# Optimization experiments

Hardware: AMD Instinct MI355X
Metric: run time of the kernel (lower is better)

The kernel has to match this reference:

```python
import jax, jax.numpy as jnp
import numpy as np

B, L, H, W = 16, 4096, 64, 64
SEQ = 1024  # target_sequence_length (hardcoded in the torch module)
SP = 32     # sqrt(SEQ)


def _conv1d(x, w, b, pad):
    y = jax.lax.conv_general_dilated(x, w, (1,), [(pad, pad)],
                                     dimension_numbers=('NCH', 'OIH', 'NCH'))
    return y + b[None, :, None]


def _conv2d(x, w, b, pad, groups=1):
    y = jax.lax.conv_general_dilated(x, w, (1, 1), [(pad, pad)] * 2,
                                     feature_group_count=groups,
                                     dimension_numbers=('NCHW', 'OIHW', 'NCHW'))
    return y + b[None, :, None, None]


def _forward(us_input, img_input, us_w1, us_b1, us_w2, us_b2, us_w3, us_b3,
             aff_w, aff_w_high, aff_thr, img_w1, img_b1, img_w2, img_b2, img_w3, img_b3,
             db_qkv_w, db_qkv_b, db_dw_w, db_dw_b, db_proj_w, db_proj_b,
             db_fc_w, db_fc_b, db_dep_w, db_dep_b, db_temp,
             ca_qkv_w, ca_qkv_b, ca_out_w, ca_out_b,
             tf_ch1_w, tf_ch1_b, tf_ch2_w, tf_ch2_b,
             tf_sp1_w, tf_sp1_b, tf_sp2_w, tf_sp2_b, cls_w, cls_b):
    b = us_input.shape[0]
    # ---- ultrasound 1D conv branch ----
    x = us_input.transpose(0, 2, 1)                    # [B,1,L]
    x = jax.nn.relu(_conv1d(x, us_w1, us_b1, 1))
    x = jax.nn.relu(_conv1d(x, us_w2, us_b2, 1))
    x = jax.nn.relu(_conv1d(x, us_w3, us_b3, 1))
    us_feat = x.transpose(0, 2, 1)                     # [B,L,64]
    # ---- adaptive frequency filtering (training-mode high-freq mask included) ----
    n = us_feat.shape[1]
    xf = jnp.fft.rfft(us_feat, axis=1, norm='ortho')   # [B,Nf,64] complex
    w_c = aff_w[:, 0] + 1j * aff_w[:, 1]
    xw = xf * w_c
    energy = jnp.sum(jnp.abs(xf) ** 2, axis=-1)        # [B,Nf]
    med = jnp.median(energy.reshape(b, -1), axis=1, keepdims=True)
    ne = energy / (med + 1e-6)
    hard = (ne > aff_thr).astype(jnp.float32)
    mask = jax.lax.stop_gradient(hard - aff_thr) + aff_thr  # straight-through threshold
    wh_c = aff_w_high[:, 0] + 1j * aff_w_high[:, 1]
    xw = xw + (xf * mask[..., None]) * wh_c
    us_feat = jnp.fft.irfft(xw, n=n, axis=1, norm='ortho')  # [B,L,64]
    # ---- image 2D conv branch ----
    y = jax.nn.relu(_conv2d(img_input, img_w1, img_b1, 1))
    y = jax.nn.relu(_conv2d(y, img_w2, img_b2, 1))
    y = jax.nn.relu(_conv2d(y, img_w3, img_b3, 1))     # [B,64,H,W]
    # ---- dual-branch feature fusion block ----
    hgt, wid = y.shape[2], y.shape[3]
    hw = hgt * wid
    qkv = jnp.einsum('oi,bihw->bohw', db_qkv_w, y) + db_qkv_b[None, :, None, None]
    qkv = _conv2d(qkv, db_dw_w, db_dw_b, 1, groups=192)      # depthwise (3x3x3 conv @ D=1 -> center 3x3)
    # convolutional branch: faithful row-major reshape as in torch
    f_all = qkv.reshape(b, hw, 12, 16).transpose(0, 2, 1, 3)  # [B,12,HW,16]
    f_all = jnp.einsum('oi,bink->bonk', db_fc_w, f_all) + db_fc_b[None, :, None, None]
    f_conv = f_all.transpose(0, 3, 1, 2).reshape(b, 144, hgt, wid)
    out_conv = _conv2d(f_conv, db_dep_w, db_dep_b, 1, groups=16)  # [B,64,H,W]
    # channel attention branch
    q, k, v = jnp.split(qkv, 3, axis=1)
    q = q.reshape(b, 4, 16, hw)
    k = k.reshape(b, 4, 16, hw)
    v = v.reshape(b, 4, 16, hw)
    q = q / jnp.maximum(jnp.linalg.norm(q, axis=-1, keepdims=True), 1e-12)
    k = k / jnp.maximum(jnp.linalg.norm(k, axis=-1, keepdims=True), 1e-12)
    attn = jax.nn.softmax(jnp.einsum('bhcn,bhdn->bhcd', q, k) * db_temp, axis=-1)
    out = jnp.einsum('bhcd,bhdn->bhcn', attn, v).reshape(b, 64, hgt, wid)
    out = jnp.einsum('oi,bihw->bohw', db_proj_w, out) + db_proj_b[None, :, None, None]
    img_feat = (out + out_conv).reshape(b, 64, hw).transpose(0, 2, 1)  # [B,HW,64]
    # ---- adaptive avg pool to SEQ (lengths divide evenly) ----
    us_red = us_feat.transpose(0, 2, 1).reshape(b, 64, SEQ, -1).mean(-1).transpose(0, 2, 1)
    img_red = img_feat.transpose(0, 2, 1).reshape(b, 64, SEQ, -1).mean(-1).transpose(0, 2, 1)
    # ---- cross-modal attention (shared qkv/out projections) ----
    def heads(t):
        u = (jnp.einsum('bli,oi->blo', t, ca_qkv_w) + ca_qkv_b).reshape(b, SEQ, 4, 3, 16)
        return (u[:, :, :, 0].transpose(0, 2, 1, 3),
                u[:, :, :, 1].transpose(0, 2, 1, 3),
                u[:, :, :, 2].transpose(0, 2, 1, 3))
    q1, k1, v1 = heads(us_red)
    q2, k2, v2 = heads(img_red)
    scale = 1.0 / jnp.sqrt(jnp.float32(16.0))
    a1 = jax.nn.softmax(jnp.einsum('bhqd,bhkd->bhqk', q1, k2) * scale, axis=-1)
    a2 = jax.nn.softmax(jnp.einsum('bhqd,bhkd->bhqk', q2, k1) * scale, axis=-1)
    o1 = jnp.einsum('bhqk,bhkd->bhqd', a1, v2).transpose(0, 2, 1, 3).reshape(b, SEQ, 64)
    o2 = jnp.einsum('bhqk,bhkd->bhqd', a2, v1).transpose(0, 2, 1, 3).reshape(b, SEQ, 64)
    o1 = jnp.einsum('bli,oi->blo', o1, ca_out_w) + ca_out_b
    o2 = jnp.einsum('bli,oi->blo', o2, ca_out_w) + ca_out_b
    t1 = o1.transpose(0, 2, 1).reshape(b, 64, SP, SP)
    t2 = o2.transpose(0, 2, 1).reshape(b, 64, SP, SP)
    # ---- modal fusion attention (channel + spatial gating) ----
    ch_pool = jnp.stack([t1.mean((2, 3)), t1.max((2, 3)), t2.mean((2, 3)), t2.max((2, 3))], axis=1)  # [B,4,64]
    c1 = _conv1d(ch_pool, tf_ch1_w, tf_ch1_b, 1)      # [B,1,64]
    c2 = _conv1d(ch_pool, tf_ch2_w, tf_ch2_b, 1)
    ch_stack = jax.nn.softmax(jnp.stack([c1, c2], 0), axis=0)      # [2,B,1,64]
    ch_stack = ch_stack.transpose(0, 1, 3, 2)[..., None]           # [2,B,64,1,1]
    sp_pool = jnp.concatenate([t1.mean(1, keepdims=True), t1.max(1, keepdims=True),
                               t2.mean(1, keepdims=True), t2.max(1, keepdims=True)], axis=1)
    s1 = _conv2d(sp_pool, tf_sp1_w, tf_sp1_b, 3)
    s2 = _conv2d(sp_pool, tf_sp2_w, tf_sp2_b, 3)
    sp_stack = jax.nn.softmax(jnp.stack([s1, s2], 0), axis=0)      # [2,B,1,SP,SP]
    att = ch_stack + sp_stack + 1.0                                # [2,B,64,SP,SP]
    fuse = att[0] * t1 + att[1] * t2
    logits = fuse.mean((2, 3)) @ cls_w.T + cls_b
    return jax.nn.softmax(logits, axis=1)


def setup_inputs() -> dict:
    key = jax.random.key(0)
    ks = iter(jax.random.split(key, 64))
    def rn(shape, s=0.2):
        return jax.random.normal(next(ks), shape, dtype=jnp.float32) * s
    d = {
        'us_input': jax.random.normal(next(ks), (B, L, 1), dtype=jnp.float32),
        'img_input': jax.random.normal(next(ks), (B, 3, H, W), dtype=jnp.float32),
        'us_w1': rn((16, 1, 3)), 'us_b1': rn((16,), 0.02),
        'us_w2': rn((32, 16, 3)), 'us_b2': rn((32,), 0.02),
        'us_w3': rn((64, 32, 3)), 'us_b3': rn((64,), 0.02),
        'aff_w': rn((64, 2), 0.02), 'aff_w_high': rn((64, 2), 0.02),
        'aff_thr': jax.random.uniform(next(ks), (1,), dtype=jnp.float32),
        'img_w1': rn((16, 3, 3, 3)), 'img_b1': rn((16,), 0.02),
        'img_w2': rn((32, 16, 3, 3)), 'img_b2': rn((32,), 0.02),
        'img_w3': rn((64, 32, 3, 3)), 'img_b3': rn((64,), 0.02),
        'db_qkv_w': rn((192, 64), 0.1), 'db_qkv_b': rn((192,), 0.02),
        'db_dw_w': rn((192, 1, 3, 3)), 'db_dw_b': rn((192,), 0.02),
        'db_proj_w': rn((64, 64), 0.1), 'db_proj_b': rn((64,), 0.02),
        'db_fc_w': rn((9, 12), 0.1), 'db_fc_b': rn((9,), 0.02),
        'db_dep_w': rn((64, 9, 3, 3), 0.1), 'db_dep_b': rn((64,), 0.02),
        'db_temp': jnp.ones((4, 1, 1), dtype=jnp.float32),
        'ca_qkv_w': rn((192, 64), 0.1), 'ca_qkv_b': rn((192,), 0.02),
        'ca_out_w': rn((64, 64), 0.1), 'ca_out_b': rn((64,), 0.02),
        'tf_ch1_w': rn((1, 4, 3)), 'tf_ch1_b': rn((1,), 0.02),
        'tf_ch2_w': rn((1, 4, 3)), 'tf_ch2_b': rn((1,), 0.02),
        'tf_sp1_w': rn((1, 4, 7, 7)), 'tf_sp1_b': rn((1,), 0.02),
        'tf_sp2_w': rn((1, 4, 7, 7)), 'tf_sp2_b': rn((1,), 0.02),
        'cls_w': rn((9, 64), 0.1), 'cls_b': rn((9,), 0.02),
    }
    return d


def reference(us_input, img_input, us_w1, us_b1, us_w2, us_b2, us_w3, us_b3,
              aff_w, aff_w_high, aff_thr, img_w1, img_b1, img_w2, img_b2, img_w3, img_b3,
              db_qkv_w, db_qkv_b, db_dw_w, db_dw_b, db_proj_w, db_proj_b,
              db_fc_w, db_fc_b, db_dep_w, db_dep_b, db_temp,
              ca_qkv_w, ca_qkv_b, ca_out_w, ca_out_b,
              tf_ch1_w, tf_ch1_b, tf_ch2_w, tf_ch2_b,
              tf_sp1_w, tf_sp1_b, tf_sp2_w, tf_sp2_b, cls_w, cls_b):
    return _forward(us_input, img_input, us_w1, us_b1, us_w2, us_b2, us_w3, us_b3,
                    aff_w, aff_w_high, aff_thr, img_w1, img_b1, img_w2, img_b2, img_w3, img_b3,
                    db_qkv_w, db_qkv_b, db_dw_w, db_dw_b, db_proj_w, db_proj_b,
                    db_fc_w, db_fc_b, db_dep_w, db_dep_b, db_temp,
                    ca_qkv_w, ca_qkv_b, ca_out_w, ca_out_b,
                    tf_ch1_w, tf_ch1_b, tf_ch2_w, tf_ch2_b,
                    tf_sp1_w, tf_sp1_b, tf_sp2_w, tf_sp2_b, cls_w, cls_b)
```

## Files before the change

kernel.cpp:

```cpp
#include <hip/hip_runtime.h>

typedef float v2f __attribute__((ext_vector_type(2)));

static constexpr size_t O_SMALL   = 0;
static constexpr size_t O_US3     = 3145728;
static constexpr size_t O_XF      = 7340032;
static constexpr size_t O_USFILT  = 11536384;
static constexpr size_t O_ENERGY  = 15730688;
static constexpr size_t O_MED     = 15764480;
static constexpr size_t O_NRM     = 15765504;
static constexpr size_t O_ATTNS   = 15767552;
static constexpr size_t O_CHPOOL  = 15783936;
static constexpr size_t O_CHW     = 15788032;
static constexpr size_t O_SPPOOL  = 15790080;
static constexpr size_t O_SPW     = 15855616;
static constexpr size_t O_QKV     = 15888384;
static constexpr size_t O_QKVDW   = 28471296;
static constexpr size_t O_OUTCONV = 41054208;
static constexpr size_t CA_USRED = 0, CA_IMGRED = 1, CA_Q1 = 2, CA_K1 = 3, CA_V1 = 4,
                        CA_Q2 = 5, CA_K2 = 6, CA_V2 = 7, CA_O1 = 8, CA_O2 = 9,
                        CA_T1 = 10, CA_T2 = 11;


template<int Ci, int Co>
// ... 56 lines not shown
    for (int i = tid; i < Ci * (TY + 2) * 64; i += 256) {
        int x  = i & 63;
        int ry = (i >> 6) % (TY + 2);
        int ci = i / ((TY + 2) * 64);
        int gy = y0 - 1 + ry;
        lds[ci][ry][x + 1] = (gy >= 0 && gy < 64) ? inb[ci * 4096 + gy * 64 + x] : 0.f;
    }
    for (int r = tid; r < Ci * (TY + 2); r += 256) {
        int ry = r % (TY + 2), ci = r / (TY + 2);
        lds[ci][ry][0] = 0.f; lds[ci][ry][65] = 0.f;
    }
    __syncthreads();
    int co   = tid / (TY * G);
    int ysub = (tid / G) % TY;
    int x0   = (tid % G) * N;
    float acc[N];
    float bias = bs[co];
#pragma unroll
    for (int j = 0; j < N; ++j) acc[j] = bias;
    const float* wb = w + co * Ci * 9;
    for (int ci = 0; ci < Ci; ++ci) {
        float wr[9];
#pragma unroll
        for (int k = 0; k < 9; ++k) wr[k] = wb[ci * 9 + k];
#pragma unroll
        for (int dy = 0; dy < 3; ++dy) {
            const float* lr = &lds[ci][ysub + dy][x0];
            float a = lr[0], bb = lr[1];
#pragma unroll
            for (int j = 0; j < N; ++j) {
                float cc = lr[2 + j];
                acc[j] += wr[dy * 3] * a + wr[dy * 3 + 1] * bb + wr[dy * 3 + 2] * cc;
                a = bb; bb = cc;
            }
        }
    }
    float* ob = out + ((size_t)b * Co + co) * 4096 + (y0 + ysub) * 64 + x0;
#pragma unroll
    for (int j = 0; j < N; ++j) ob[j] = fmaxf(acc[j], 0.f);
}

__device__ __forceinline__ void fft4096_r4_sb(float2* A, int tid)
{
    int Ns = 1;
    for (int s = 0; s < 6; ++s) {
        float cfac = -0.25f / (float)Ns;
        float2 va[4][4];
#pragma unroll
        for (int r = 0; r < 4; ++r) {
            int j = (r << 8) + tid;
            va[r][0] = A[j];
            va[r][1] = A[j + 1024];
            va[r][2] = A[j + 2048];
            va[r][3] = A[j + 3072];
        }
        __syncthreads();
#pragma unroll
        for (int r = 0; r < 4; ++r) {
            int j = (r << 8) + tid;
            int jm = j & (Ns - 1);
            float rev = (float)jm * cfac;
            float s1 = __builtin_amdgcn_sinf(rev);
            float c1 = __builtin_amdgcn_cosf(rev);
            float c2 = c1 * c1 - s1 * s1, s2 = 2.f * c1 * s1;
            float c3 = c2 * c1 - s2 * s1, s3 = c2 * s1 + s2 * c1;
            float2 v0 = va[r][0], v1 = va[r][1], v2 = va[r][2], v3 = va[r][3];
            float2 u1 = make_float2(v1.x * c1 - v1.y * s1, v1.x * s1 + v1.y * c1);
            float2 u2 = make_float2(v2.x * c2 - v2.y * s2, v2.x * s2 + v2.y * c2);
            float2 u3 = make_float2(v3.x * c3 - v3.y * s3, v3.x * s3 + v3.y * c3);
            float t0x = v0.x + u2.x, t0y = v0.y + u2.y;
            float t1x = v0.x - u2.x, t1y = v0.y - u2.y;
            float t2x = u1.x + u3.x, t2y = u1.y + u3.y;
            float t3x = u1.x - u3.x, t3y = u1.y - u3.y;
            int base = ((j - jm) << 2) + jm;
            A[base]          = make_float2(t0x + t2x, t0y + t2y);
            A[base + Ns]     = make_float2(t1x + t3y, t1y - t3x);
            A[base + 2 * Ns] = make_float2(t0x - t2x, t0y - t2y);
            A[base + 3 * Ns] = make_float2(t1x - t3y, t1y + t3x);
        }
        __syncthreads();
        Ns <<= 2;
    }
}

__device__ __forceinline__ void fft_fwd_body(char* smem_raw, int row,
    const float* __restrict__ us3, float* __restrict__ xf)
{
    float2* A = (float2*)smem_raw;
    int tid = threadIdx.x;
    const float* x = us3 + (size_t)row * 4096;
    for (int r = 0; r < 16; ++r) {
        int i = (r << 8) + tid;
        A[i] = make_float2(x[i], 0.f);
    }
    __syncthreads();
    fft4096_r4_sb(A, tid);
    float* out = xf + (size_t)row * 4098;
    for (int r = 0; r < 9; ++r) {
        int f = (r << 8) + tid;
        if (f < 2049) {
            out[2 * f]     = A[f].x * (1.f / 64.f);
            out[2 * f + 1] = A[f].y * (1.f / 64.f);
        }
    }
}

__device__ __forceinline__ void energy_body(int bid,
    const float* __restrict__ xf, float* __restrict__ energy)
{
    int idx = bid * 256 + threadIdx.x;
    if (idx >= 16 * 2049) return;
    int b = idx / 2049, f = idx % 2049;
    const float* p = xf + (size_t)b * 64 * 4098 + 2 * f;
    float e = 0.f;
    for (int ch = 0; ch < 64; ++ch) {
        float re = p[0], im = p[1];
        e += re * re + im * im;
        p += 4098;
    }
    energy[idx] = e;
}

__device__ __forceinline__ void median_body(char* smem_raw, int b,
    const float* __restrict__ energy, float* __restrict__ med)
{
    float* s = (float*)smem_raw;
    int tid = threadIdx.x;
    for (int r = 0; r < 16; ++r) {
        int i = (r << 8) + tid;
        s[i] = (i < 2049) ? energy[b * 2049 + i] : 3.0e38f;
    }
    __syncthreads();
    for (int k = 2; k <= 4096; k <<= 1) {
        for (int j = k >> 1; j > 0; j >>= 1) {
            for (int r = 0; r < 16; ++r) {
                int i = (r << 8) + tid;
                int ixj = i ^ j;
                if (ixj > i) {
                    bool up = ((i & k) == 0);
                    float a = s[i], bb = s[ixj];
                    if ((a > bb) == up) { s[i] = bb; s[ixj] = a; }
                }
            }
            __syncthreads();
        }
    }
    if (tid == 0) med[b] = s[1024];
}

__device__ __forceinline__ void filter_ifft_body(char* smem_raw, int row,
    const float* __restrict__ xf, const float* __restrict__ energy,
    const float* __restrict__ med, const float* __restrict__ aff_w,
    const float* __restrict__ aff_wh, const float* __restrict__ thr_p,
    float* __restrict__ us_filt)
{
    float2* A = (float2*)smem_raw;
    int b = row >> 6, ch = row & 63;
    int tid = threadIdx.x;
    float thr = thr_p[0];
    float mden = med[b] + 1e-6f;
    float w0r = aff_w[2 * ch], w0i = aff_w[2 * ch + 1];
    float whr = aff_wh[2 * ch], whi = aff_wh[2 * ch + 1];
    const float* X = xf + (size_t)row * 4098;
    const float* E = energy + b * 2049;
    for (int r = 0; r < 9; ++r) {
        int f = (r << 8) + tid;
        if (f < 2049) {
            float re = X[2 * f], im = X[2 * f + 1];
            float mask = (E[f] / mden > thr) ? 1.f : 0.f;
            float wr = w0r + mask * whr;
            float wi = w0i + mask * whi;
            float xr = re * wr - im * wi;
            float xi = re * wi + im * wr;
            A[f] = make_float2(xr, -xi);
            if (f >= 1 && f <= 2047) A[4096 - f] = make_float2(xr, xi);
        }
    }
    __syncthreads();
    fft4096_r4_sb(A, tid);
    float* out = us_filt + (size_t)row * 4096;
    for (int r = 0; r < 16; ++r) {
        int i = (r << 8) + tid;
        out[i] = A[i].x * (1.f / 64.f);
    }
}

__device__ __forceinline__ void qkv1x1_body(int bid, const float* __restrict__ y,
    const float* __restrict__ w, const float* __restrict__ bs, float* __restrict__ out)
{
    int oc = bid & 3;
    int pc = (bid >> 2) & 15;
    int b  = bid >> 6;
    int p = pc * 256 + threadIdx.x;
    const float* inb = y + (size_t)b * 262144 + p;
    v2f reg[32];
#pragma unroll
    for (int ci = 0; ci < 32; ++ci) {
        v2f r; r.x = inb[(2 * ci) * 4096]; r.y = inb[(2 * ci + 1) * 4096];
        reg[ci] = r;
    }
    float* ob = out + (size_t)b * 786432 + (size_t)oc * 48 * 4096 + p;
    for (int o = 0; o < 48; ++o) {
        const v2f* wr = (const v2f*)(w + (oc * 48 + o) * 64);
        v2f s2 = {0.f, 0.f};
#pragma unroll
        for (int ci = 0; ci < 32; ++ci) s2 = wr[ci] * reg[ci] + s2;
        ob[o * 4096] = bs[oc * 48 + o] + s2.x + s2.y;
    }
}

__device__ __forceinline__ void dwconv_body(int bid, const float* __restrict__ in,
    const float* __restrict__ w, const float* __restrict__ bs, float* __restrict__ out)
{
    int idx = bid * 256 + threadIdx.x;
    int x = idx & 63, yy = (idx >> 6) & 63;
    int c = (idx >> 12) % 192;
    const float* p = in + idx;
    const float* wp = w + c * 9;
    float acc = bs[c];
    bool ym = yy > 0, yp = yy < 63, xm = x > 0, xp = x < 63;
    float s = wp[4] * p[0];
    if (ym) { s += wp[1] * p[-64]; if (xm) s += wp[0] * p[-65]; if (xp) s += wp[2] * p[-63]; }
    if (xm) s += wp[3] * p[-1];
    if (xp) s += wp[5] * p[1];
    if (yp) { s += wp[7] * p[64];  if (xm) s += wp[6] * p[63];  if (xp) s += wp[8] * p[65]; }
    out[idx] = acc + s;
}

__device__ __forceinline__ void fc_body(int bid, const float* __restrict__ qkv_dw,
    const float* __restrict__ fw, const float* __restrict__ fb, float* __restrict__ fcv)
{
    int idx = bid * 256 + threadIdx.x;
    int k = idx & 15;
    int p = (idx >> 4) & 4095;
    int b = idx >> 16;
    const float* base = qkv_dw + (size_t)b * 786432;
    float u[12];
#pragma unroll
    for (int i = 0; i < 12; ++i) u[i] = base[p * 192 + i * 16 + k];
#pragma unroll
    for (int o = 0; o < 9; ++o) {
        float s = fb[o];
#pragma unroll
        for (int i = 0; i < 12; ++i) s += fw[o * 12 + i] * u[i];
        fcv[(((size_t)b * 16 + k) * 9 + o) * 4096 + p] = s;
    }
}

__device__ __forceinline__ void depconv2_body(char* smem_raw, int bid,
    const float* __restrict__ fcv, const float* __restrict__ w,
    const float* __restrict__ bs, float* __restrict__ out)
{
    auto lds = (float(*)[10][66])smem_raw;
    int band = bid & 7;
    int g    = (bid >> 3) & 15;
    int b    = bid >> 7;
    int y0 = band * 8;
    int tid = threadIdx.x;
    const float* inb = fcv + ((size_t)(b * 16 + g) * 9) * 4096;
    for (int i = tid; i < 9 * 10 * 64; i += 256) {
        int x  = i & 63;
        int ry = (i >> 6) % 10;
        int ci = i / 640;
        int gy = y0 - 1 + ry;
        lds[ci][ry][x + 1] = (gy >= 0 && gy < 64) ? inb[ci * 4096 + gy * 64 + x] : 0.f;
    }
    for (int i = tid; i < 90; i += 256) {
        int ry = i % 10, ci = i / 10;
        lds[ci][ry][0] = 0.f; lds[ci][ry][65] = 0.f;
    }
    __syncthreads();
    int co   = tid >> 6;
    int ysub = (tid >> 3) & 7;
    int x0   = (tid & 7) * 8;
    int ocg  = g * 4 + co;
    float acc[8];
    float bias = bs[ocg];
#pragma unroll
    for (int j = 0; j < 8; ++j) acc[j] = bias;
    const float* wb = w + ocg * 81;
    for (int ci = 0; ci < 9; ++ci) {
        float wr[9];
#pragma unroll
        for (int k = 0; k < 9; ++k) wr[k] = wb[ci * 9 + k];
#pragma unroll
        for (int dy = 0; dy < 3; ++dy) {
            const float* lr = &lds[ci][ysub + dy][x0];
            float a = lr[0], bb = lr[1];
#pragma unroll
            for (int j = 0; j < 8; ++j) {
                float cc = lr[2 + j];
                acc[j] += wr[dy * 3] * a + wr[dy * 3 + 1] * bb + wr[dy * 3 + 2] * cc;
                a = bb; bb = cc;
            }
        }
    }
    float* ob = out + ((size_t)b * 64 + ocg) * 4096 + (y0 + ysub) * 64 + x0;
#pragma unroll
    for (int j = 0; j < 8; ++j) ob[j] = acc[j];
}

__device__ __forceinline__ void qknorm_body(char* smem_raw, int row,
    const float* __restrict__ qkv_dw, float* __restrict__ nrm)
{
    float* red = (float*)smem_raw;
    int which = row >> 10;
    int r = row & 1023;
    int b = r >> 6, hd = r & 63;
    const float* p = qkv_dw + ((size_t)b * 192 + which * 64 + hd) * 4096;
    float s = 0.f;
    for (int i = threadIdx.x; i < 4096; i += 256) { float v = p[i]; s += v * v; }
    red[threadIdx.x] = s;
    __syncthreads();
    for (int st = 128; st > 0; st >>= 1) {
        if (threadIdx.x < st) red[threadIdx.x] += red[threadIdx.x + st];
        __syncthreads();
    }
    if (threadIdx.x == 0) nrm[row] = sqrtf(red[0]);
}

__device__ __forceinline__ void chan_attn_part_body(char* smem_raw, int blk,
    const float* __restrict__ qkv_dw, float* __restrict__ part)
{
    auto Qs  = (float(*)[130])smem_raw;
    auto Ks2 = (float(*)[130])(smem_raw + 16 * 130 * 4);
    int nc = blk & 7;
    int bh = blk >> 3;
    int b = bh >> 2, h = bh & 3;
    int c = threadIdx.x >> 4, d = threadIdx.x & 15;
    const float* qbase = qkv_dw + ((size_t)b * 192 + h * 16) * 4096 + nc * 512;
    const float* kbase = qkv_dw + ((size_t)b * 192 + 64 + h * 16) * 4096 + nc * 512;
    float s = 0.f;
    for (int n0 = 0; n0 < 512; n0 += 128) {
        __syncthreads();
        for (int r = 0; r < 8; ++r) {
            int i = (r << 8) + threadIdx.x;
// ... 15 lines not shown
    int b  = bid >> 4;
    int wave = threadIdx.x >> 6, lane = threadIdx.x & 63;
    int c = rg * 4 + wave;
    const float* p1 = t1 + ((size_t)b * 64 + c) * 1024;
    const float* p2 = t2 + ((size_t)b * 64 + c) * 1024;
    float m1 = 0.f, x1 = -3e38f, m2 = 0.f, x2 = -3e38f;
#pragma unroll
    for (int i = 0; i < 16; ++i) {
        int p = lane + i * 64;
        float a = p1[p], bb = p2[p];
        m1 += a; x1 = fmaxf(x1, a);
        m2 += bb; x2 = fmaxf(x2, bb);
    }
    for (int off = 32; off > 0; off >>= 1) {
        m1 += __shfl_xor(m1, off);
        x1 = fmaxf(x1, __shfl_xor(x1, off));
        m2 += __shfl_xor(m2, off);
        x2 = fmaxf(x2, __shfl_xor(x2, off));
    }
    if (lane == 0) {
        chpool[b * 256 + c]       = m1 * (1.f / 1024.f);
        chpool[b * 256 + 64 + c]  = x1;
        chpool[b * 256 + 128 + c] = m2 * (1.f / 1024.f);
        chpool[b * 256 + 192 + c] = x2;
    }
}

__device__ __forceinline__ void sppool_body(int bid, const float* __restrict__ t1,
    const float* __restrict__ t2, float* __restrict__ sppool)
{
    int b = bid >> 2;
    int p = (bid & 3) * 256 + threadIdx.x;
    float m1 = 0.f, x1 = -3e38f, m2 = 0.f, x2 = -3e38f;
    const float* p1 = t1 + (size_t)b * 65536 + p;
    const float* p2 = t2 + (size_t)b * 65536 + p;
    for (int c = 0; c < 64; ++c) {
        float a = p1[c * 1024], bb = p2[c * 1024];
        m1 += a; x1 = fmaxf(x1, a);
        m2 += bb; x2 = fmaxf(x2, bb);
    }
    sppool[b * 4096 + p]        = m1 * (1.f / 64.f);
    sppool[b * 4096 + 1024 + p] = x1;
    sppool[b * 4096 + 2048 + p] = m2 * (1.f / 64.f);
    sppool[b * 4096 + 3072 + p] = x2;
}

__device__ __forceinline__ void chgate_body(int b, const float* __restrict__ chpool,
    const float* __restrict__ w1, const float* __restrict__ b1,
    const float* __restrict__ w2, const float* __restrict__ b2, float* __restrict__ chw)
{
    int c = threadIdx.x;
    if (c >= 64) return;
    float a1 = b1[0], a2 = b2[0];
    for (int ic = 0; ic < 4; ++ic) {
        const float* cp = chpool + b * 256 + ic * 64;
        for (int d = -1; d <= 1; ++d) {
            int cc = c + d;
            if (cc >= 0 && cc < 64) {
                a1 += w1[ic * 3 + d + 1] * cp[cc];
                a2 += w2[ic * 3 + d + 1] * cp[cc];
            }
        }
    }
    float mx = fmaxf(a1, a2);
    float e1 = __expf(a1 - mx), e2 = __expf(a2 - mx);
    float inv = 1.f / (e1 + e2);
    chw[b * 64 + c]        = e1 * inv;
    chw[1024 + b * 64 + c] = e2 * inv;
}

__device__ __forceinline__ void spgate_body(int bid, const float* __restrict__ sppool,
    const float* __restrict__ w1, const float* __restrict__ b1,
    const float* __restrict__ w2, const float* __restrict__ b2, float* __restrict__ spw)
{
    int idx = bid * 256 + threadIdx.x;
    int p = idx & 1023;
    int b = idx >> 10;
    int y = p >> 5, x = p & 31;
    float a1 = b1[0], a2 = b2[0];
    for (int ic = 0; ic < 4; ++ic) {
        const float* sp = sppool + b * 4096 + ic * 1024;
        for (int dy = -3; dy <= 3; ++dy) {
            int yy = y + dy;
            if (yy < 0 || yy > 31) continue;
            for (int dx = -3; dx <= 3; ++dx) {
                int xx = x + dx;
                if (xx < 0 || xx > 31) continue;
                float v = sp[yy * 32 + xx];
                int wi = ic * 49 + (dy + 3) * 7 + (dx + 3);
                a1 += w1[wi] * v;
                a2 += w2[wi] * v;
            }
        }
    }
    float mx = fmaxf(a1, a2);
    float e1 = __expf(a1 - mx), e2 = __expf(a2 - mx);
    float inv = 1.f / (e1 + e2);
    spw[idx]         = e1 * inv;
    spw[16384 + idx] = e2 * inv;
}


__global__ __launch_bounds__(256) void s1_kernel(const float* us_in, const float* uw, const float* ub,
    float* uo, const float* iin, const float* iw, const float* ib, float* io)
{
    __shared__ __align__(16) char smem[3168];
    if (blockIdx.x < 512) conv1d3_body<1, 16>(smem, blockIdx.x, us_in, uw, ub, uo);
    else                  conv2d3_body<3, 16, 2>(smem, blockIdx.x - 512, iin, iw, ib, io);
}

__global__ __launch_bounds__(256) void s2_kernel(const float* ui, const float* uw, const float* ub,
    float* uo, const float* ii, const float* iw, const float* ib, float* io)
{
    __shared__ __align__(16) char smem[16896];
    if (blockIdx.x < 512) conv1d3_body<16, 32>(smem, blockIdx.x, ui, uw, ub, uo);
    else                  conv2d3_body<16, 32, 2>(smem, blockIdx.x - 512, ii, iw, ib, io);
}

__global__ __launch_bounds__(256) void s3_kernel(const float* ui, const float* uw, const float* ub,
    float* uo, const float* ii, const float* iw, const float* ib, float* io)
{
    __shared__ __align__(16) char smem[33792];
    if (blockIdx.x < 512) conv1d3_body<32, 64>(smem, blockIdx.x, ui, uw, ub, uo);
    else                  conv2d3_body<32, 64, 2>(smem, blockIdx.x - 512, ii, iw, ib, io);
}

__global__ __launch_bounds__(256) void s4_kernel(const float* us3, float* xf,
    const float* y, const float* qw, const float* qb, float* qkv)
{
    __shared__ __align__(16) char smem[32768];
    if (blockIdx.x < 1024) fft_fwd_body(smem, blockIdx.x, us3, xf);
    else                   qkv1x1_body(blockIdx.x - 1024, y, qw, qb, qkv);
}

__global__ __launch_bounds__(256) void s5_kernel(const float* qkv, const float* dww,
    const float* dwb, float* qkv_dw, const float* xf, float* energy)
{
    if (blockIdx.x < 49152) dwconv_body(blockIdx.x, qkv, dww, dwb, qkv_dw);
    else                    energy_body(blockIdx.x - 49152, xf, energy);
}

__global__ __launch_bounds__(256) void s6_kernel(const float* qkv_dw, const float* fw,
    const float* fb, float* fcv, const float* energy, float* med, float* part)
{
    __shared__ __align__(16) char smem[16640];
    if (blockIdx.x < 4096)      fc_body(blockIdx.x, qkv_dw, fw, fb, fcv);
    else if (blockIdx.x < 4112) median_body(smem, blockIdx.x - 4096, energy, med);
    else                        chan_attn_part_body(smem, blockIdx.x - 4112, qkv_dw, part);
}

__global__ __launch_bounds__(256) void s7_kernel(const float* fcv, const float* dw,
    const float* db, float* out_conv, const float* qkv_dw, float* nrm,
    const float* xf, const float* energy, const float* med, const float* aw,
    const float* awh, const float* thr, float* us_filt)
{
    __shared__ __align__(16) char smem[32768];
    if (blockIdx.x < 2048)      depconv2_body(smem, blockIdx.x, fcv, dw, db, out_conv);
    else if (blockIdx.x < 4096) qknorm_body(smem, blockIdx.x - 2048, qkv_dw, nrm);
    else                        filter_ifft_body(smem, blockIdx.x - 4096, xf, energy, med, aw, awh, thr, us_filt);
}

__global__ __launch_bounds__(256) void zero_kernel(float* o1t, float* o2t, float* lsg)
{
    int idx = blockIdx.x * 256 + threadIdx.x;
    if (idx < 1048576) { o1t[idx] = 0.f; o2t[idx] = 0.f; }
    if (idx < 131072) lsg[idx] = 0.f;
}

__global__ __launch_bounds__(256) void s16_kernel(const float* t1, const float* t2,
    float* chpool, float* sppool)
{
    if (blockIdx.x < 256) chpool2_body(blockIdx.x, t1, t2, chpool);
    else                  sppool_body(blockIdx.x - 256, t1, t2, sppool);
}

__global__ __launch_bounds__(256) void s17_kernel(const float* sppool, const float* sw1,
    const float* sb1, const float* sw2, const float* sb2, float* spw,
    const float* chpool, const float* cw1, const float* cb1, const float* cw2,
    const float* cb2, float* chw)
{
    if (blockIdx.x < 64) spgate_body(blockIdx.x, sppool, sw1, sb1, sw2, sb2, spw);
    else                 chgate_body(blockIdx.x - 64, chpool, cw1, cb1, cw2, cb2, chw);
}

__global__ __launch_bounds__(256) void chan_attn_merge_kernel(
    const float* __restrict__ part, const float* __restrict__ nrm,
    const float* __restrict__ temp, float* __restrict__ attn_s)
{
    int bh = blockIdx.x;
    int b = bh >> 2, h = bh & 3;
    int c = threadIdx.x >> 4, d = threadIdx.x & 15;
    float s = 0.f;
#pragma unroll
    for (int i = 0; i < 8; ++i) s += part[(size_t)(bh * 8 + i) * 256 + threadIdx.x];
    float nq = fmaxf(nrm[b * 64 + h * 16 + c], 1e-12f);
    float nk = fmaxf(nrm[1024 + b * 64 + h * 16 + d], 1e-12f);
    s = s / (nq * nk) * temp[h];
    __shared__ float S[16][17];
    S[c][d] = s;
    __syncthreads();
    if (threadIdx.x < 16) {
        int cc = threadIdx.x;
        float mx = -3e30f;
        for (int dd = 0; dd < 16; ++dd) mx = fmaxf(mx, S[cc][dd]);
        float sm = 0.f;
        float e[16];
        for (int dd = 0; dd < 16; ++dd) { e[dd] = __expf(S[cc][dd] - mx); sm += e[dd]; }
        float inv = 1.f / sm;
        float* dst = attn_s + (size_t)bh * 256 + cc * 16;
        for (int dd = 0; dd < 16; ++dd) dst[dd] = e[dd] * inv;
    }
}


__global__ __launch_bounds__(256, 2) void attnproj_kernel(const float* __restrict__ attn_s,
    const float* __restrict__ qkv_dw, const float* __restrict__ outconv,
    const float* __restrict__ pw, const float* __restrict__ pb, float* __restrict__ img_feat)
{
    int blk = blockIdx.x;
    int oc = blk & 1;
    int pc = (blk >> 1) & 15;
    int b  = blk >> 5;
    int n = pc * 256 + threadIdx.x;
    const float* vb = qkv_dw + ((size_t)b * 192 + 128) * 4096 + n;
    v2f v[32];
#pragma unroll
    for (int i = 0; i < 32; ++i) {
        v2f r; r.x = vb[(2 * i) * 4096]; r.y = vb[(2 * i + 1) * 4096];
        v[i] = r;
    }
    const float* ab = attn_s + (size_t)b * 1024;
    for (int h = 0; h < 4; ++h) {
        v2f tmp[8];
#pragma unroll
        for (int c2 = 0; c2 < 8; ++c2) {
            v2f s2a = {0.f, 0.f}, s2b = {0.f, 0.f};
            const v2f* r0 = (const v2f*)(ab + (h * 16 + 2 * c2) * 16);
            const v2f* r1 = (const v2f*)(ab + (h * 16 + 2 * c2 + 1) * 16);
#pragma unroll
            for (int d2 = 0; d2 < 8; ++d2) {
                s2a = r0[d2] * v[h * 8 + d2] + s2a;
                s2b = r1[d2] * v[h * 8 + d2] + s2b;
            }
            v2f t; t.x = s2a.x + s2a.y; t.y = s2b.x + s2b.y;
            tmp[c2] = t;
        }
#pragma unroll
        for (int c2 = 0; c2 < 8; ++c2) v[h * 8 + c2] = tmp[c2];
    }
    float* ofb = img_feat + (size_t)b * 262144 + (size_t)oc * 32 * 4096 + n;
    const float* ocb = outconv + (size_t)b * 262144 + (size_t)oc * 32 * 4096 + n;
    for (int o = 0; o < 32; ++o) {
        const v2f* wr = (const v2f*)(pw + (oc * 32 + o) * 64);
        v2f s2 = {0.f, 0.f};
#pragma unroll
        for (int c2 = 0; c2 < 32; ++c2) s2 = wr[c2] * v[c2] + s2;
        ofb[o * 4096] = pb[oc * 32 + o] + ocb[o * 4096] + s2.x + s2.y;
    }
}

__global__ __launch_bounds__(256) void poolred_kernel(const float* __restrict__ us_filt,
    const float* __restrict__ img_feat, float* __restrict__ us_redT, float* __restrict__ img_redT)
{
    int idx = blockIdx.x * 256 + threadIdx.x;
    int s4 = idx & 1023;
    int c = (idx >> 10) & 63;
    int b = (idx >> 16) & 15;
    int m = idx >> 20;
    const float* in = (m ? img_feat : us_filt) + ((size_t)b * 64 + c) * 4096 + s4 * 4;
    float4 v4 = *(const float4*)in;
    float v = 0.25f * (v4.x + v4.y + v4.z + v4.w);
    (m ? img_redT : us_redT)[((size_t)b * 64 + c) * 1024 + s4] = v;
}

__global__ __launch_bounds__(256, 2) void caqkv2_kernel(const float* __restrict__ us_redT,
    const float* __restrict__ img_redT, const float* __restrict__ qw, const float* __restrict__ qb,
    float* __restrict__ q1, float* __restrict__ k1, float* __restrict__ v1,
    float* __restrict__ q2, float* __restrict__ k2, float* __restrict__ v2)
{
    int blk = blockIdx.x;
    int h  = blk & 3;
    int pc = (blk >> 2) & 3;
    int b  = (blk >> 4) & 15;
    int m  = blk >> 8;
    int l = pc * 256 + threadIdx.x;
    const float* in = (m ? img_redT : us_redT) + (size_t)b * 65536 + l;
    v2f reg[32];
#pragma unroll
    for (int i = 0; i < 32; ++i) {
        v2f r; r.x = in[(2 * i) * 1024]; r.y = in[(2 * i + 1) * 1024];
        reg[i] = r;
    }
    size_t rowoff = ((size_t)(b * 4 + h) * 1024 + l) * 16;
    float* dst[3] = { (m ? q2 : q1) + rowoff, (m ? k2 : k1) + rowoff, (m ? v2 : v1) + rowoff };
#pragma unroll
    for (int which = 0; which < 3; ++which) {
        float* dp = dst[which];
        for (int d = 0; d < 16; ++d) {
            int o = h * 48 + which * 16 + d;
            const v2f* wr = (const v2f*)(qw + o * 64);
            v2f s2 = {0.f, 0.f};
#pragma unroll
            for (int i = 0; i < 32; ++i) s2 = wr[i] * reg[i] + s2;
            dp[d] = qb[o] + s2.x + s2.y;
        }
    }
}

__global__ __launch_bounds__(256) void kmax_kernel(const float* __restrict__ k1,
    const float* __restrict__ k2, float* __restrict__ kmax)
{
    int unit = blockIdx.x;
    int h = unit & 3, m = (unit >> 2) & 1, b = unit >> 3;
    const float* K = m ? k1 : k2;
    const float* Kb = K + (size_t)(b * 4 + h) * 16384;
    int tid = threadIdx.x;
    float mx = 0.f;
#pragma unroll
    for (int j = 0; j < 4; ++j) {
        const float* kp = Kb + (size_t)(tid + 256 * j) * 16;
        float s = 0.f;
#pragma unroll
        for (int d = 0; d < 16; ++d) s += kp[d] * kp[d];
        mx = fmaxf(mx, s);
    }
    for (int off = 32; off > 0; off >>= 1) mx = fmaxf(mx, __shfl_xor(mx, off));
    __shared__ float red[4];
    if ((tid & 63) == 0) red[tid >> 6] = mx;
    __syncthreads();
    if (tid == 0) {
        float r = fmaxf(fmaxf(red[0], red[1]), fmaxf(red[2], red[3]));
        kmax[unit] = sqrtf(r);
    }
}

__global__ __launch_bounds__(256, 2) void cross_attn9_kernel(
    const float* __restrict__ q1, const float* __restrict__ k1, const float* __restrict__ v1,
    const float* __restrict__ q2, const float* __restrict__ k2, const float* __restrict__ v2,
    const float* __restrict__ kmax, float* __restrict__ ls_glob,
    float* __restrict__ o1t, float* __restrict__ o2t)
{
    int blk  = blockIdx.x;
    int kt   = blk & 7;
    int unit = blk >> 3;
    int h = unit & 3;
    int m = (unit >> 2) & 1;
    int b = unit >> 3;
    const float* Q = m ? q2 : q1;
    const float* K = m ? k1 : k2;
    const float* V = m ? v1 : v2;
    const float* Qb = Q + (size_t)(b * 4 + h) * 16384;
    const float* Kb = K + (size_t)(b * 4 + h) * 16384 + kt * 128 * 16;
    const float* Vb = V + (size_t)(b * 4 + h) * 16384 + kt * 128 * 16;
    int tid = threadIdx.x;
    const float SC = 0.25f * 1.44269504088896340736f;
    float km = kmax[unit];
    v2f qr[4][8], acc[4][8];
    float M[4], ls[4];
#pragma unroll
    for (int j = 0; j < 4; ++j) {
        const v2f* qp = (const v2f*)(Qb + (size_t)(tid + 256 * j) * 16);
        v2f qs2 = {0.f, 0.f};
#pragma unroll
        for (int i = 0; i < 8; ++i) {
            v2f q = qp[i];
            qs2 = q * q + qs2;
            qr[j][i] = q * SC;
        }
        M[j] = sqrtf(qs2.x + qs2.y) * km * SC;
        ls[j] = 0.f;
#pragma unroll
        for (int i = 0; i < 8; ++i) acc[j][i] = (v2f){0.f, 0.f};
    }
    __shared__ float Ks[64 * 16];
    __shared__ float Vs[64 * 16];
    for (int t0 = 0; t0 < 128; t0 += 64) {
        __syncthreads();
        ((float4*)Ks)[tid] = ((const float4*)(Kb + t0 * 16))[tid];
        ((float4*)Vs)[tid] = ((const float4*)(Vb + t0 * 16))[tid];
        __syncthreads();
#pragma unroll 2
        for (int t = 0; t < 64; ++t) {
            const v2f* k2p = (const v2f*)&Ks[t * 16];
            v2f kk[8];
#pragma unroll
            for (int i = 0; i < 8; ++i) kk[i] = k2p[i];
            float p[4];
#pragma unroll
            for (int j = 0; j < 4; ++j) {
                v2f s2 = {0.f, 0.f};
#pragma unroll
                for (int i = 0; i < 8; ++i) s2 = qr[j][i] * kk[i] + s2;
                p[j] = exp2f(s2.x + s2.y - M[j]);
                ls[j] += p[j];
            }
            const v2f* v2p = (const v2f*)&Vs[t * 16];
            v2f vv[8];
#pragma unroll
            for (int i = 0; i < 8; ++i) vv[i] = v2p[i];
#pragma unroll
            for (int j = 0; j < 4; ++j) {
                v2f pj = {p[j], p[j]};
#pragma unroll
                for (int i = 0; i < 8; ++i) acc[j][i] = pj * vv[i] + acc[j][i];
            }
        }
    }
    float* obase = (m ? o2t : o1t) + (size_t)b * 65536 + (size_t)(h * 16) * 1024;
#pragma unroll
    for (int j = 0; j < 4; ++j) {
        int q = tid + 256 * j;
        atomicAdd(&ls_glob[(size_t)unit * 1024 + q], ls[j]);
        float* onum = obase + q;
#pragma unroll
        for (int i = 0; i < 8; ++i) {
            atomicAdd(&onum[(2 * i) * 1024], acc[j][i].x);
            atomicAdd(&onum[(2 * i + 1) * 1024], acc[j][i].y);
        }
    }
}

__global__ __launch_bounds__(256, 2) void caout3_kernel(const float* __restrict__ o1t,
    const float* __restrict__ o2t, const float* __restrict__ ls_glob,
    const float* __restrict__ ow, const float* __restrict__ ob_,
    float* __restrict__ t1, float* __restrict__ t2)
{
    int blk = blockIdx.x;
    int oc = blk & 1;
    int pc = (blk >> 1) & 3;
    int b  = (blk >> 3) & 15;
    int m  = blk >> 7;
    int l = pc * 256 + threadIdx.x;
    float inv[4];
#pragma unroll
    for (int h = 0; h < 4; ++h)
        inv[h] = 1.f / ls_glob[(size_t)(b * 8 + m * 4 + h) * 1024 + l];
    const float* in = (m ? o2t : o1t) + (size_t)b * 65536 + l;
    v2f reg[32];
#pragma unroll
    for (int i = 0; i < 32; ++i) {
        float iv = inv[i >> 3];
        v2f r; r.x = in[(2 * i) * 1024] * iv; r.y = in[(2 * i + 1) * 1024] * iv;
        reg[i] = r;
    }
    float* t = (m ? t2 : t1) + (size_t)b * 65536 + (size_t)oc * 32 * 1024 + l;
    for (int o = 0; o < 32; ++o) {
        const v2f* wr = (const v2f*)(ow + (oc * 32 + o) * 64);
        v2f s2 = {0.f, 0.f};
#pragma unroll
        for (int i = 0; i < 32; ++i) s2 = wr[i] * reg[i] + s2;
        t[o * 1024] = ob_[oc * 32 + o] + s2.x + s2.y;
    }
}

__global__ __launch_bounds__(256) void final2_kernel(const float* __restrict__ t1,
    const float* __restrict__ t2, const float* __restrict__ chw, const float* __restrict__ spw,
    const float* __restrict__ clsw, const float* __restrict__ clsb, float* __restrict__ out)
{
    int b = blockIdx.x;
    int wave = threadIdx.x >> 6, lane = threadIdx.x & 63;
    __shared__ float feat[64];
    __shared__ float lg[9];
    const float* s1 = spw + b * 1024;
    const float* s2 = spw + 16384 + b * 1024;
    for (int round = 0; round < 16; ++round) {
        int c = round * 4 + wave;
        float g1 = chw[b * 64 + c] + 1.f;
        float g2 = chw[1024 + b * 64 + c] + 1.f;
        const float* p1 = t1 + ((size_t)b * 64 + c) * 1024;
        const float* p2 = t2 + ((size_t)b * 64 + c) * 1024;
        float acc = 0.f;
#pragma unroll
        for (int i = 0; i < 16; ++i) {
            int p = lane + i * 64;
            acc += (g1 + s1[p]) * p1[p] + (g2 + s2[p]) * p2[p];
        }
        for (int off = 32; off > 0; off >>= 1) acc += __shfl_xor(acc, off);
        if (lane == 0) feat[c] = acc * (1.f / 1024.f);
    }
    __syncthreads();
    if (threadIdx.x < 9) {
        int c = threadIdx.x;
        float s = clsb[c];
        for (int i = 0; i < 64; ++i) s += clsw[c * 64 + i] * feat[i];
        lg[c] = s;
    }
    __syncthreads();
    if (threadIdx.x == 0) {
        float mx = -3e38f;
        for (int o = 0; o < 9; ++o) mx = fmaxf(mx, lg[o]);
        float sm = 0.f;
        float e[9];
        for (int o = 0; o < 9; ++o) { e[o] = __expf(lg[o] - mx); sm += e[o]; }
        float inv = 1.f / sm;
        for (int o = 0; o < 9; ++o) out[b * 9 + o] = e[o] * inv;
    }
}

extern "C" void kernel_launch(void* const* d_in, const int* in_sizes, int n_in,
                              void* d_out, int out_size, void* d_ws, size_t ws_size,
                              hipStream_t stream)
{
    (void)in_sizes; (void)n_in; (void)out_size; (void)ws_size;
    const float* us_input = (const float*)d_in[0];
    const float* img_input = (const float*)d_in[1];
    const float* us_w1 = (const float*)d_in[2];  const float* us_b1 = (const float*)d_in[3];
    const float* us_w2 = (const float*)d_in[4];  const float* us_b2 = (const float*)d_in[5];
    const float* us_w3 = (const float*)d_in[6];  const float* us_b3 = (const float*)d_in[7];
    const float* aff_w = (const float*)d_in[8];  const float* aff_wh = (const float*)d_in[9];
    const float* aff_thr = (const float*)d_in[10];
    const float* img_w1 = (const float*)d_in[11]; const float* img_b1 = (const float*)d_in[12];
    const float* img_w2 = (const float*)d_in[13]; const float* img_b2 = (const float*)d_in[14];
    const float* img_w3 = (const float*)d_in[15]; const float* img_b3 = (const float*)d_in[16];
    const float* db_qkv_w = (const float*)d_in[17]; const float* db_qkv_b = (const float*)d_in[18];
    const float* db_dw_w = (const float*)d_in[19];  const float* db_dw_b = (const float*)d_in[20];
    const float* db_proj_w = (const float*)d_in[21]; const float* db_proj_b = (const float*)d_in[22];
    const float* db_fc_w = (const float*)d_in[23];  const float* db_fc_b = (const float*)d_in[24];
    const float* db_dep_w = (const float*)d_in[25]; const float* db_dep_b = (const float*)d_in[26];
    const float* db_temp = (const float*)d_in[27];
    const float* ca_qkv_w = (const float*)d_in[28]; const float* ca_qkv_b = (const float*)d_in[29];
    const float* ca_out_w = (const float*)d_in[30]; const float* ca_out_b = (const float*)d_in[31];
    const float* tf_ch1_w = (const float*)d_in[32]; const float* tf_ch1_b = (const float*)d_in[33];
    const float* tf_ch2_w = (const float*)d_in[34]; const float* tf_ch2_b = (const float*)d_in[35];
    const float* tf_sp1_w = (const float*)d_in[36]; const float* tf_sp1_b = (const float*)d_in[37];
    const float* tf_sp2_w = (const float*)d_in[38]; const float* tf_sp2_b = (const float*)d_in[39];
    const float* cls_w = (const float*)d_in[40];   const float* cls_b = (const float*)d_in[41];

    float* ws = (float*)d_ws;
    float* us1     = ws + O_SMALL;
    float* us2     = ws + O_SMALL + 1048576;
    float* us3     = ws + O_US3;
    float* xf      = ws + O_XF;
    float* us_filt = ws + O_USFILT;
    float* energy  = ws + O_ENERGY;
    float* med     = ws + O_MED;
    float* nrm     = ws + O_NRM;
    float* attn_s  = ws + O_ATTNS;
    float* chpool  = ws + O_CHPOOL;
    float* chw     = ws + O_CHW;
    float* sppool  = ws + O_SPPOOL;
    float* spw     = ws + O_SPW;
    float* qkv     = ws + O_QKV;
    float* qkv_dw  = ws + O_QKVDW;
    float* out_conv= ws + O_OUTCONV;
    float* img1 = ws + O_USFILT;
    float* img2 = ws + O_USFILT + 1048576;
    float* y = ws + O_QKVDW;
    float* fcv = qkv;
    float* img_feat = xf;
    float* ca_part = ws + O_SMALL;
    float* us_redT  = ws + O_QKV + CA_USRED  * 1048576;
    float* img_redT = ws + O_QKV + CA_IMGRED * 1048576;
    float* q1 = ws + O_QKV + CA_Q1 * 1048576;
    float* k1 = ws + O_QKV + CA_K1 * 1048576;
    float* v1 = ws + O_QKV + CA_V1 * 1048576;
    float* q2 = ws + O_QKV + CA_Q2 * 1048576;
    float* k2 = ws + O_QKV + CA_K2 * 1048576;
    float* v2 = ws + O_QKV + CA_V2 * 1048576;
    float* o1t = ws + O_QKV + CA_O1 * 1048576;
    float* o2t = ws + O_QKV + CA_O2 * 1048576;
    float* t1 = ws + O_QKV + CA_T1 * 1048576;
    float* t2 = ws + O_QKV + CA_T2 * 1048576;
    float* ca_ls   = ws + O_US3;
    float* ca_kmax = ws + O_US3 + 1048576;

    s1_kernel<<<1024, 256, 0, stream>>>(us_input, us_w1, us_b1, us1,
                                        img_input, img_w1, img_b1, img1);
    s2_kernel<<<1024, 256, 0, stream>>>(us1, us_w2, us_b2, us2,
                                        img1, img_w2, img_b2, img2);
    s3_kernel<<<1024, 256, 0, stream>>>(us2, us_w3, us_b3, us3,
                                        img2, img_w3, img_b3, y);
    s4_kernel<<<2048, 256, 0, stream>>>(us3, xf, y, db_qkv_w, db_qkv_b, qkv);
    s5_kernel<<<49281, 256, 0, stream>>>(qkv, db_dw_w, db_dw_b, qkv_dw, xf, energy);
    s6_kernel<<<4624, 256, 0, stream>>>(qkv_dw, db_fc_w, db_fc_b, fcv, energy, med, ca_part);
    s7_kernel<<<5120, 256, 0, stream>>>(fcv, db_dep_w, db_dep_b, out_conv,
                                        qkv_dw, nrm, xf, energy, med,
                                        aff_w, aff_wh, aff_thr, us_filt);
    zero_kernel<<<4096, 256, 0, stream>>>(o1t, o2t, ca_ls);
    chan_attn_merge_kernel<<<64, 256, 0, stream>>>(ca_part, nrm, db_temp, attn_s);
    attnproj_kernel<<<512, 256, 0, stream>>>(attn_s, qkv_dw, out_conv, db_proj_w, db_proj_b, img_feat);
    poolred_kernel<<<8192, 256, 0, stream>>>(us_filt, img_feat, us_redT, img_redT);
    caqkv2_kernel<<<512, 256, 0, stream>>>(us_redT, img_redT, ca_qkv_w, ca_qkv_b,
                                           q1, k1, v1, q2, k2, v2);
    kmax_kernel<<<128, 256, 0, stream>>>(k1, k2, ca_kmax);
    cross_attn9_kernel<<<1024, 256, 0, stream>>>(q1, k1, v1, q2, k2, v2, ca_kmax,
                                                 ca_ls, o1t, o2t);
    caout3_kernel<<<256, 256, 0, stream>>>(o1t, o2t, ca_ls, ca_out_w, ca_out_b, t1, t2);
    s16_kernel<<<320, 256, 0, stream>>>(t1, t2, chpool, sppool);
    s17_kernel<<<80, 256, 0, stream>>>(sppool, tf_sp1_w, tf_sp1_b, tf_sp2_w, tf_sp2_b, spw,
                                       chpool, tf_ch1_w, tf_ch1_b, tf_ch2_w, tf_ch2_b, chw);
    final2_kernel<<<16, 256, 0, stream>>>(t1, t2, chw, spw, cls_w, cls_b, (float*)d_out);
}
```

Measured before the change: 865.5 us.

## Fuse pooling into iFFT and attnproj epilogues, fold kmax into caqkv

The 4:1 average pooling now happens inside the filter/iFFT epilogue and inside attnproj, using a wave shuffle there. This removes the separate poolred kernel and the full-resolution us_filt and img_feat round trips. The key-norm max is computed in caqkv2 with a wave reduction and a float-as-uint atomicMax, which removes the kmax kernel; zero_kernel now clears the new atomic buffer. Workspace buffers are relocated to fit. The cost is extra shuffles and atomics, plus a dependence on non-negative floats ordering correctly as unsigned integers.

```diff
diff --git a/kernel.cpp b/kernel.cpp
--- a/kernel.cpp
+++ b/kernel.cpp
@@ -232,7 +232,7 @@
     const float* __restrict__ xf, const float* __restrict__ energy,
     const float* __restrict__ med, const float* __restrict__ aff_w,
     const float* __restrict__ aff_wh, const float* __restrict__ thr_p,
-    float* __restrict__ us_filt)
+    float* __restrict__ us_redT)
 {
     float2* A = (float2*)smem_raw;
     int b = row >> 6, ch = row & 63;
@@ -258,10 +258,13 @@
     }
     __syncthreads();
     fft4096_r4_sb(A, tid);
-    float* out = us_filt + (size_t)row * 4096;
-    for (int r = 0; r < 16; ++r) {
-        int i = (r << 8) + tid;
-        out[i] = A[i].x * (1.f / 64.f);
+    float* outp = us_redT + (size_t)row * 1024;
+    const float SCL = 0.25f * (1.f / 64.f);
+#pragma unroll
+    for (int r = 0; r < 4; ++r) {
+        int s4 = (r << 8) + tid;
+        float v = (A[4 * s4].x + A[4 * s4 + 1].x + A[4 * s4 + 2].x + A[4 * s4 + 3].x) * SCL;
+        outp[s4] = v;
     }
 }
 
@@ -583,19 +586,21 @@
 __global__ __launch_bounds__(256) void s7_kernel(const float* fcv, const float* dw,
     const float* db, float* out_conv, const float* qkv_dw, float* nrm,
     const float* xf, const float* energy, const float* med, const float* aw,
-    const float* awh, const float* thr, float* us_filt)
+    const float* awh, const float* thr, float* us_redT)
 {
     __shared__ __align__(16) char smem[32768];
     if (blockIdx.x < 2048)      depconv2_body(smem, blockIdx.x, fcv, dw, db, out_conv);
     else if (blockIdx.x < 4096) qknorm_body(smem, blockIdx.x - 2048, qkv_dw, nrm);
-    else                        filter_ifft_body(smem, blockIdx.x - 4096, xf, energy, med, aw, awh, thr, us_filt);
-}
-
-__global__ __launch_bounds__(256) void zero_kernel(float* o1t, float* o2t, float* lsg)
+    else                        filter_ifft_body(smem, blockIdx.x - 4096, xf, energy, med, aw, awh, thr, us_redT);
+}
+
+__global__ __launch_bounds__(256) void zero_kernel(float* o1t, float* o2t, float* lsg,
+                                                   unsigned* kmax2)
 {
     int idx = blockIdx.x * 256 + threadIdx.x;
     if (idx < 1048576) { o1t[idx] = 0.f; o2t[idx] = 0.f; }
     if (idx < 131072) lsg[idx] = 0.f;
+    if (idx < 128) kmax2[idx] = 0u;
 }
 
 __global__ __launch_bounds__(256) void s16_kernel(const float* t1, const float* t2,
@@ -646,13 +651,14 @@
 
 __global__ __launch_bounds__(256, 2) void attnproj_kernel(const float* __restrict__ attn_s,
     const float* __restrict__ qkv_dw, const float* __restrict__ outconv,
-    const float* __restrict__ pw, const float* __restrict__ pb, float* __restrict__ img_feat)
+    const float* __restrict__ pw, const float* __restrict__ pb, float* __restrict__ img_redT)
 {
     int blk = blockIdx.x;
     int oc = blk & 1;
     int pc = (blk >> 1) & 15;
     int b  = blk >> 5;
-    int n = pc * 256 + threadIdx.x;
+    int tid = threadIdx.x;
+    int n = pc * 256 + tid;
     const float* vb = qkv_dw + ((size_t)b * 192 + 128) * 4096 + n;
     v2f v[32];
 #pragma unroll
@@ -679,35 +685,25 @@
 #pragma unroll
         for (int c2 = 0; c2 < 8; ++c2) v[h * 8 + c2] = tmp[c2];
     }
-    float* ofb = img_feat + (size_t)b * 262144 + (size_t)oc * 32 * 4096 + n;
     const float* ocb = outconv + (size_t)b * 262144 + (size_t)oc * 32 * 4096 + n;
+    float* orow = img_redT + ((size_t)b * 64 + (size_t)oc * 32) * 1024 + (n >> 2);
     for (int o = 0; o < 32; ++o) {
         const v2f* wr = (const v2f*)(pw + (oc * 32 + o) * 64);
         v2f s2 = {0.f, 0.f};
 #pragma unroll
         for (int c2 = 0; c2 < 32; ++c2) s2 = wr[c2] * v[c2] + s2;
-        ofb[o * 4096] = pb[oc * 32 + o] + ocb[o * 4096] + s2.x + s2.y;
-    }
-}
-
-__global__ __launch_bounds__(256) void poolred_kernel(const float* __restrict__ us_filt,
-    const float* __restrict__ img_feat, float* __restrict__ us_redT, float* __restrict__ img_redT)
-{
-    int idx = blockIdx.x * 256 + threadIdx.x;
-    int s4 = idx & 1023;
-    int c = (idx >> 10) & 63;
-    int b = (idx >> 16) & 15;
-    int m = idx >> 20;
-    const float* in = (m ? img_feat : us_filt) + ((size_t)b * 64 + c) * 4096 + s4 * 4;
-    float4 v4 = *(const float4*)in;
-    float v = 0.25f * (v4.x + v4.y + v4.z + v4.w);
-    (m ? img_redT : us_redT)[((size_t)b * 64 + c) * 1024 + s4] = v;
+        float val = pb[oc * 32 + o] + ocb[o * 4096] + s2.x + s2.y;
+        float s = val + __shfl_xor(val, 1);
+        s += __shfl_xor(s, 2);
+        if ((tid & 3) == 0) orow[(size_t)o * 1024] = s * 0.25f;
+    }
 }
 
 __global__ __launch_bounds__(256, 2) void caqkv2_kernel(const float* __restrict__ us_redT,
     const float* __restrict__ img_redT, const float* __restrict__ qw, const float* __restrict__ qb,
     float* __restrict__ q1, float* __restrict__ k1, float* __restrict__ v1,
-    float* __restrict__ q2, float* __restrict__ k2, float* __restrict__ v2)
+    float* __restrict__ q2, float* __restrict__ k2, float* __restrict__ v2,
+    unsigned* __restrict__ kmax2)
 {
     int blk = blockIdx.x;
     int h  = blk & 3;
@@ -724,6 +720,7 @@
     }
     size_t rowoff = ((size_t)(b * 4 + h) * 1024 + l) * 16;
     float* dst[3] = { (m ? q2 : q1) + rowoff, (m ? k2 : k1) + rowoff, (m ? v2 : v1) + rowoff };
+    float knorm2 = 0.f;
 #pragma unroll
     for (int which = 0; which < 3; ++which) {
         float* dp = dst[which];
@@ -733,42 +730,23 @@
             v2f s2 = {0.f, 0.f};
 #pragma unroll
             for (int i = 0; i < 32; ++i) s2 = wr[i] * reg[i] + s2;
-            dp[d] = qb[o] + s2.x + s2.y;
-        }
-    }
-}
-
-__global__ __launch_bounds__(256) void kmax_kernel(const float* __restrict__ k1,
-    const float* __restrict__ k2, float* __restrict__ kmax)
-{
-    int unit = blockIdx.x;
-    int h = unit & 3, m = (unit >> 2) & 1, b = unit >> 3;
-    const float* K = m ? k1 : k2;
-    const float* Kb = K + (size_t)(b * 4 + h) * 16384;
-    int tid = threadIdx.x;
-    float mx = 0.f;
-#pragma unroll
-    for (int j = 0; j < 4; ++j) {
-        const float* kp = Kb + (size_t)(tid + 256 * j) * 16;
-        float s = 0.f;
-#pragma unroll
-        for (int d = 0; d < 16; ++d) s += kp[d] * kp[d];
-        mx = fmaxf(mx, s);
-    }
-    for (int off = 32; off > 0; off >>= 1) mx = fmaxf(mx, __shfl_xor(mx, off));
-    __shared__ float red[4];
-    if ((tid & 63) == 0) red[tid >> 6] = mx;
-    __syncthreads();
-    if (tid == 0) {
-        float r = fmaxf(fmaxf(red[0], red[1]), fmaxf(red[2], red[3]));
-        kmax[unit] = sqrtf(r);
+            float val = qb[o] + s2.x + s2.y;
+            dp[d] = val;
+            if (which == 1) knorm2 += val * val;
+        }
+    }
+    for (int off = 32; off > 0; off >>= 1)
+        knorm2 = fmaxf(knorm2, __shfl_xor(knorm2, off));
+    if ((threadIdx.x & 63) == 0) {
+        int unit = b * 8 + (1 - m) * 4 + h;
+        atomicMax(&kmax2[unit], __float_as_uint(knorm2));
     }
 }
 
 __global__ __launch_bounds__(256, 2) void cross_attn9_kernel(
     const float* __restrict__ q1, const float* __restrict__ k1, const float* __restrict__ v1,
     const float* __restrict__ q2, const float* __restrict__ k2, const float* __restrict__ v2,
-    const float* __restrict__ kmax, float* __restrict__ ls_glob,
+    const unsigned* __restrict__ kmax2, float* __restrict__ ls_glob,
     float* __restrict__ o1t, float* __restrict__ o2t)
 {
     int blk  = blockIdx.x;
@@ -785,7 +763,7 @@
     const float* Vb = V + (size_t)(b * 4 + h) * 16384 + kt * 128 * 16;
     int tid = threadIdx.x;
     const float SC = 0.25f * 1.44269504088896340736f;
-    float km = kmax[unit];
+    float km = sqrtf(__uint_as_float(kmax2[unit]));
     v2f qr[4][8], acc[4][8];
     float M[4], ls[4];
 #pragma unroll
@@ -962,7 +940,6 @@
     float* us2     = ws + O_SMALL + 1048576;
     float* us3     = ws + O_US3;
     float* xf      = ws + O_XF;
-    float* us_filt = ws + O_USFILT;
     float* energy  = ws + O_ENERGY;
     float* med     = ws + O_MED;
     float* nrm     = ws + O_NRM;
@@ -978,10 +955,11 @@
     float* img2 = ws + O_USFILT + 1048576;
     float* y = ws + O_QKVDW;
     float* fcv = qkv;
-    float* img_feat = xf;
     float* ca_part = ws + O_SMALL;
-    float* us_redT  = ws + O_QKV + CA_USRED  * 1048576;
-    float* img_redT = ws + O_QKV + CA_IMGRED * 1048576;
+    float* ca_ls    = ws + O_US3;
+    unsigned* ca_kmax2 = (unsigned*)(ws + O_US3 + 131072);
+    float* us_redT  = ws + O_US3 + 262144;
+    float* img_redT = ws + O_US3 + 1310720;
     float* q1 = ws + O_QKV + CA_Q1 * 1048576;
     float* k1 = ws + O_QKV + CA_K1 * 1048576;
     float* v1 = ws + O_QKV + CA_V1 * 1048576;
@@ -992,8 +970,6 @@
     float* o2t = ws + O_QKV + CA_O2 * 1048576;
     float* t1 = ws + O_QKV + CA_T1 * 1048576;
     float* t2 = ws + O_QKV + CA_T2 * 1048576;
-    float* ca_ls   = ws + O_US3;
-    float* ca_kmax = ws + O_US3 + 1048576;
 
     s1_kernel<<<1024, 256, 0, stream>>>(us_input, us_w1, us_b1, us1,
                                         img_input, img_w1, img_b1, img1);
@@ -1006,15 +982,13 @@
     s6_kernel<<<4624, 256, 0, stream>>>(qkv_dw, db_fc_w, db_fc_b, fcv, energy, med, ca_part);
     s7_kernel<<<5120, 256, 0, stream>>>(fcv, db_dep_w, db_dep_b, out_conv,
                                         qkv_dw, nrm, xf, energy, med,
-                                        aff_w, aff_wh, aff_thr, us_filt);
-    zero_kernel<<<4096, 256, 0, stream>>>(o1t, o2t, ca_ls);
+                                        aff_w, aff_wh, aff_thr, us_redT);
+    zero_kernel<<<4096, 256, 0, stream>>>(o1t, o2t, ca_ls, ca_kmax2);
     chan_attn_merge_kernel<<<64, 256, 0, stream>>>(ca_part, nrm, db_temp, attn_s);
-    attnproj_kernel<<<512, 256, 0, stream>>>(attn_s, qkv_dw, out_conv, db_proj_w, db_proj_b, img_feat);
-    poolred_kernel<<<8192, 256, 0, stream>>>(us_filt, img_feat, us_redT, img_redT);
+    attnproj_kernel<<<512, 256, 0, stream>>>(attn_s, qkv_dw, out_conv, db_proj_w, db_proj_b, img_redT);
     caqkv2_kernel<<<512, 256, 0, stream>>>(us_redT, img_redT, ca_qkv_w, ca_qkv_b,
-                                           q1, k1, v1, q2, k2, v2);
-    kmax_kernel<<<128, 256, 0, stream>>>(k1, k2, ca_kmax);
-    cross_attn9_kernel<<<1024, 256, 0, stream>>>(q1, k1, v1, q2, k2, v2, ca_kmax,
+                                           q1, k1, v1, q2, k2, v2, ca_kmax2);
+    cross_attn9_kernel<<<1024, 256, 0, stream>>>(q1, k1, v1, q2, k2, v2, ca_kmax2,
                                                  ca_ls, o1t, o2t);
     caout3_kernel<<<256, 256, 0, stream>>>(o1t, o2t, ca_ls, ca_out_w, ca_out_b, t1, t2);
     s16_kernel<<<320, 256, 0, stream>>>(t1, t2, chpool, sppool);
```

Measured after the change: 871.7 us. About the same (+0.7%).
